# Kernel tuning notes

Measured on AMD Instinct MI355X. Metric: run time of the kernel, lower is better.

## Reference

```python
import jax, jax.numpy as jnp
import numpy as np

B, S, HID = 4, 2048, 768
NH = 12
HD = HID // NH  # 64


def setup_inputs() -> dict:
    key = jax.random.key(0)
    ks = jax.random.split(key, 8)
    scale = 1.0 / np.sqrt(HID)
    return {
        "hidden_states": jax.random.normal(ks[0], (B, S, HID), dtype=jnp.float32),
        "attention_mask": jnp.zeros((B, 1, 1, S), dtype=jnp.float32),
        "Wq": jax.random.normal(ks[1], (HID, HID), dtype=jnp.float32) * scale,
        "bq": jnp.zeros((HID,), dtype=jnp.float32),
        "Wk": jax.random.normal(ks[2], (HID, HID), dtype=jnp.float32) * scale,
        "bk": jnp.zeros((HID,), dtype=jnp.float32),
        "Wv": jax.random.normal(ks[3], (HID, HID), dtype=jnp.float32) * scale,
        "bv": jnp.zeros((HID,), dtype=jnp.float32),
    }


def _split_heads(x):
    # [B, S, HID] -> [B, NH, S, HD]
    return x.reshape(B, S, NH, HD).transpose(0, 2, 1, 3)


def reference(hidden_states, attention_mask, Wq, bq, Wk, bk, Wv, bv):
    q = _split_heads(hidden_states @ Wq + bq)
    k = _split_heads(hidden_states @ Wk + bk)
    v = _split_heads(hidden_states @ Wv + bv)
    # scores: [B, NH, S, S]
    scores = jnp.einsum("bhqd,bhkd->bhqk", q, k) / jnp.sqrt(jnp.float32(HD))
    scores = scores + attention_mask  # additive mask, broadcast [B,1,1,S]
    probs = jax.nn.softmax(scores, axis=-1)
    ctx = jnp.einsum("bhqk,bhkd->bhqd", probs, v)
    # [B, NH, S, HD] -> [B, S, HID]
    return ctx.transpose(0, 2, 1, 3).reshape(B, S, HID)
```

## Files before the change

kernel.cpp:

```cpp
#include <hip/hip_runtime.h>
#include <hip/hip_bf16.h>
#include <math.h>

#define B_ 4
#define S_ 2048
#define HID_ 768
#define NH_ 12
#define HD_ 64

typedef short bf16x8 __attribute__((ext_vector_type(8)));
typedef short bf16x4 __attribute__((ext_vector_type(4)));
typedef float f32x4 __attribute__((ext_vector_type(4)));
typedef unsigned short u16;
typedef unsigned int uu32;

#define QSCALE 0.18033688011112042f
#define LOG2E  1.4426950408889634f

__device__ __forceinline__ u16 f2bf(float f) {
  union { float f; unsigned u; } x; x.f = f;
  unsigned u = x.u;
  u += 0x7FFFu + ((u >> 16) & 1u);
  return (u16)(u >> 16);
}

__device__ __forceinline__ float exp2_fast(float x) {
  float r;
  asm("v_exp_f32 %0, %1" : "=v"(r) : "v"(x));
  return r;
}

__device__ __forceinline__ uu32 cvt_pk_bf16(float lo, float hi) {
  uu32 r;
  asm("v_cvt_pk_bf16_f32 %0, %1, %2" : "=v"(r) : "v"(lo), "v"(hi));
  return r;
}

__global__ void prep(const float* __restrict__ x, u16* __restrict__ xb,
                     const float* __restrict__ m, float* __restrict__ emf,
                     u16* __restrict__ emp,
                     const float* __restrict__ Wq, const float* __restrict__ Wk,
                     const float* __restrict__ Wv, u16* __restrict__ wt) {
  __shared__ float t[32][33];
  int bid = blockIdx.x;
  int tid = threadIdx.x;
  if (bid < 6144) {
    int i = (bid * 256 + tid) * 4;
    float4 v = *(const float4*)(x + i);
    ushort4 o;
    o.x = f2bf(v.x); o.y = f2bf(v.y); o.z = f2bf(v.z); o.w = f2bf(v.w);
    *(ushort4*)(xb + i) = o;
  } else if (bid < 6176) {
    int i = (bid - 6144) * 256 + tid;
    float e = exp2f(m[i] * LOG2E);
    emf[i] = e;
    int j = i & 63;
    int p = (j & 32) | (((j >> 2) & 3) << 3) | (((j >> 4) & 1) << 2) | (j & 3);
    emp[(i & ~63) | p] = f2bf(e);
  } else {
    int r = bid - 6176;
    int z = r / 576; r %= 576;
    int by = r / 24, bx = r % 24;
    const float* W = z == 0 ? Wq : (z == 1 ? Wk : Wv);
    u16* out = wt + (size_t)z * HID_ * HID_;
    int tx = tid & 31, ty = tid >> 5;
    int k0 = bx * 32, n0 = by * 32;
#pragma unroll
    for (int i = 0; i < 4; i++)
      t[ty + 8 * i][tx] = W[(k0 + ty + 8 * i) * HID_ + n0 + tx];
    __syncthreads();
#pragma unroll
    for (int i = 0; i < 4; i++)
      out[(n0 + ty + 8 * i) * HID_ + k0 + tx] = f2bf(t[tx][ty + 8 * i]);
  }
}

__global__ __launch_bounds__(256) void qkv_gemm4(
    const u16* __restrict__ xb, const u16* __restrict__ wt_all,
    const float* __restrict__ bq, const float* __restrict__ bk,
    const float* __restrict__ bv, const float* __restrict__ emf,
    u16* __restrict__ q, u16* __restrict__ k_, u16* __restrict__ vt) {
  int id = blockIdx.x;
  int xcd = id & 7, ii = id >> 3;
  int bx = xcd * 8 + (ii & 7);
  int by = ii >> 3;
  int z = by / 6;
  const float* bias = z == 0 ? bq : (z == 1 ? bk : bv);

  int tid = threadIdx.x;
  int l = tid & 63, w = tid >> 6;
  int lr = l & 15, lg = l >> 4;
  int wm = w >> 1, wn = w & 1;

  __shared__ __align__(16) u16 Al[2][128 * 40];
  __shared__ __align__(16) u16 Bl[2][128 * 40];

  const u16* Ab = xb + (size_t)bx * 128 * 768;
  const u16* Bb = wt_all + (size_t)by * 128 * 768;

  int sr = tid >> 1, sc = (tid & 1) * 2;
  const u16* ag = Ab + sr * 768 + sc * 8;
  const u16* bg = Bb + sr * 768 + sc * 8;
  int woff = sr * 40 + sc * 8;

  int aoff[4], boff[4];
#pragma unroll
  for (int mt = 0; mt < 4; mt++)
    aoff[mt] = (64 * wm + 16 * mt + lr) * 40 + lg * 8;
#pragma unroll
  for (int nt = 0; nt < 4; nt++)
    boff[nt] = (64 * wn + 16 * nt + lr) * 40 + lg * 8;

  bf16x8 sA0, sA1, sB0, sB1;

  sA0 = *(const bf16x8*)(ag);
  sA1 = *(const bf16x8*)(ag + 8);
  sB0 = *(const bf16x8*)(bg);
  sB1 = *(const bf16x8*)(bg + 8);
  *(bf16x8*)(&Al[0][woff]) = sA0;
  *(bf16x8*)(&Al[0][woff + 8]) = sA1;
  *(bf16x8*)(&Bl[0][woff]) = sB0;
  *(bf16x8*)(&Bl[0][woff + 8]) = sB1;
  __syncthreads();

  f32x4 acc[4][4] = {};

  auto body = [&](int buf, int t) {
    int k0 = (t + 1) * 32;
    sA0 = *(const bf16x8*)(ag + k0);
    sA1 = *(const bf16x8*)(ag + k0 + 8);
    sB0 = *(const bf16x8*)(bg + k0);
    sB1 = *(const bf16x8*)(bg + k0 + 8);

    bf16x8 af[4], bf[4];
#pragma unroll
    for (int mt = 0; mt < 4; mt++)
      af[mt] = *(const bf16x8*)(&Al[buf][aoff[mt]]);
#pragma unroll
    for (int nt = 0; nt < 4; nt++)
      bf[nt] = *(const bf16x8*)(&Bl[buf][boff[nt]]);
#pragma unroll
    for (int mt = 0; mt < 4; mt++)
#pragma unroll
      for (int nt = 0; nt < 4; nt++)
        acc[mt][nt] = __builtin_amdgcn_mfma_f32_16x16x32_bf16(af[mt], bf[nt], acc[mt][nt], 0, 0, 0);

    int nb = buf ^ 1;
    *(bf16x8*)(&Al[nb][woff]) = sA0;
    *(bf16x8*)(&Al[nb][woff + 8]) = sA1;
    *(bf16x8*)(&Bl[nb][woff]) = sB0;
    *(bf16x8*)(&Bl[nb][woff + 8]) = sB1;
    __syncthreads();
  };

#pragma unroll 1
  for (int tt = 0; tt < 11; ++tt) {
    body(0, 2 * tt);
    body(1, 2 * tt + 1);
  }
  body(0, 22);
  {
    bf16x8 af[4], bf[4];
#pragma unroll
    for (int mt = 0; mt < 4; mt++)
      af[mt] = *(const bf16x8*)(&Al[1][aoff[mt]]);
#pragma unroll
    for (int nt = 0; nt < 4; nt++)
      bf[nt] = *(const bf16x8*)(&Bl[1][boff[nt]]);
#pragma unroll
    for (int mt = 0; mt < 4; mt++)
#pragma unroll
      for (int nt = 0; nt < 4; nt++)
        acc[mt][nt] = __builtin_amdgcn_mfma_f32_16x16x32_bf16(af[mt], bf[nt], acc[mt][nt], 0, 0, 0);
  }

  int hh = 2 * (by % 6) + wn;
  int mbase = bx * 128 + 64 * wm;
  int bidx = mbase >> 11;
  float osc = z == 0 ? QSCALE : 1.0f;
#pragma unroll
  for (int mt = 0; mt < 4; mt++)
#pragma unroll
    for (int nt = 0; nt < 4; nt++) {
      int d = 16 * nt + lr;
      float bval = bias[(by % 6) * 128 + 64 * wn + d];
      int s = (mbase + 16 * mt + 4 * lg) & 2047;
      if (z == 2) {
        f32x4 emv = *(const f32x4*)(emf + (size_t)bidx * S_ + s);
        ushort4 pk;
        pk.x = f2bf((acc[mt][nt][0] + bval) * emv[0]);
        pk.y = f2bf((acc[mt][nt][1] + bval) * emv[1]);
        pk.z = f2bf((acc[mt][nt][2] + bval) * emv[2]);
        pk.w = f2bf((acc[mt][nt][3] + bval) * emv[3]);
        *(ushort4*)(vt + ((size_t)(bidx * NH_ + hh) * HD_ + d) * S_ + s) = pk;
      } else {
        u16* o = z == 0 ? q : k_;
#pragma unroll
        for (int r = 0; r < 4; r++)
          o[((size_t)(bidx * NH_ + hh) * S_ + s + r) * HD_ + d] =
              f2bf((acc[mt][nt][r] + bval) * osc);
      }
    }
}

__global__ __launch_bounds__(256) void attn9(
    const u16* __restrict__ q, const u16* __restrict__ k_,
    const u16* __restrict__ vt, const u16* __restrict__ emp,
    float* __restrict__ out) {
  int id = blockIdx.x;
  int xcd = id & 7, ii = id >> 3;
  int bh = xcd * 6 + (ii >> 4);
  int qb = ii & 15;
  int tid = threadIdx.x;
  int l = tid & 63, w = tid >> 6;
  int lr = l & 15, lg = l >> 4;
  int bidx = bh / NH_, h = bh % NH_;
  int q0 = qb * 128 + w * 32;

  __shared__ __align__(16) u16 Kl[2][64 * 64];
  __shared__ __align__(16) u16 Vl[2][64 * 64];
  __shared__ __align__(16) u16 El[2][16 * 64];

  {
    bf16x8 z = {};
    *(bf16x8*)(&El[0][0] + tid * 8) = z;
  }

  const u16* qbase = q + ((size_t)bh * S_ + q0) * HD_;
  const u16* kbase = k_ + (size_t)bh * S_ * HD_;
  const u16* vtb = vt + (size_t)bh * HD_ * S_;
  const u16* emb = emp + (size_t)bidx * S_;

  bf16x8 aq[2][2];
#pragma unroll
  for (int qt = 0; qt < 2; qt++)
#pragma unroll
    for (int h2 = 0; h2 < 2; h2++)
      aq[qt][h2] = *(const bf16x8*)(qbase + (size_t)(16 * qt + lr) * HD_ + 8 * lg + 32 * h2);

  f32x4 ctx[2][4] = {};
  f32x4 lsum[2] = {};

  int i0 = tid, i1 = tid + 256;
  int r0 = i0 >> 3, c0 = i0 & 7, r1 = i1 >> 3, c1 = i1 & 7;
  int kw0 = r0 * 64 + ((c0 ^ (r0 & 7)) << 3);
  int kw1 = r1 * 64 + ((c1 ^ (r1 & 7)) << 3);
  int w1_0 = 32 * (c0 >> 2) + 16 * (c0 & 1) + 4 * ((c0 >> 1) & 1);
  int w1_1 = 32 * (c1 >> 2) + 16 * (c1 & 1) + 4 * ((c1 >> 1) & 1);
  int vw0a = r0 * 64 + ((((w1_0 >> 3) ^ (r0 & 7)) << 3) | (w1_0 & 7));
  int vw0b = r0 * 64 + (((((w1_0 >> 3) + 1) ^ (r0 & 7)) << 3) | (w1_0 & 7));
  int vw1a = r1 * 64 + ((((w1_1 >> 3) ^ (r1 & 7)) << 3) | (w1_1 & 7));
  int vw1b = r1 * 64 + (((((w1_1 >> 3) + 1) ^ (r1 & 7)) << 3) | (w1_1 & 7));

  int sw = lr & 7;
  int off[4][2], eoff[2];
#pragma unroll
  for (int nt = 0; nt < 4; nt++)
#pragma unroll
    for (int hf = 0; hf < 2; hf++)
      off[nt][hf] = (16 * nt + lr) * 64 + (((hf * 4 + lg) ^ sw) << 3);
#pragma unroll
  for (int hf = 0; hf < 2; hf++)
    eoff[hf] = lr * 64 + (((hf * 4 + lg) ^ sw) << 3);

  bf16x8 sK0, sK1, sV0, sV1, sE;

  auto stage_load = [&](int kt) {
    const u16* kp = kbase + (size_t)kt * 64 * HD_;
    sK0 = *(const bf16x8*)(kp + i0 * 8);
    sK1 = *(const bf16x8*)(kp + i1 * 8);
    const u16* vp = vtb + kt * 64;
    sV0 = *(const bf16x8*)(vp + (size_t)r0 * S_ + c0 * 8);
    sV1 = *(const bf16x8*)(vp + (size_t)r1 * S_ + c1 * 8);
    if (tid < 8) sE = *(const bf16x8*)(emb + kt * 64 + tid * 8);
  };
  auto stage_write = [&](int buf) {
    u16* Kb = &Kl[buf][0];
    u16* Vb = &Vl[buf][0];
    *(bf16x8*)(Kb + kw0) = sK0;
    *(bf16x8*)(Kb + kw1) = sK1;
    union { bf16x8 v; bf16x4 hh[2]; } uv0, uv1;
    uv0.v = sV0; uv1.v = sV1;
    *(bf16x4*)(Vb + vw0a) = uv0.hh[0];
    *(bf16x4*)(Vb + vw0b) = uv0.hh[1];
    *(bf16x4*)(Vb + vw1a) = uv1.hh[0];
    *(bf16x4*)(Vb + vw1b) = uv1.hh[1];
    if (tid < 8) *(bf16x8*)(&El[buf][0] + tid * 8) = sE;
  };

  auto body = [&](int buf, int it) {
    stage_load((it + 1) & 31);

    const u16* Kp = &Kl[buf][0];
    const u16* Vp = &Vl[buf][0];
    const u16* Ep = &El[buf][0];

    bf16x8 kf[4][2];
#pragma unroll
    for (int nt = 0; nt < 4; nt++) {
      kf[nt][0] = *(const bf16x8*)(Kp + off[nt][0]);
      kf[nt][1] = *(const bf16x8*)(Kp + off[nt][1]);
    }

    f32x4 sc[2][4] = {};
    __builtin_amdgcn_s_setprio(1);
#pragma unroll
    for (int nt = 0; nt < 4; nt++)
#pragma unroll
      for (int qt = 0; qt < 2; qt++) {
        sc[qt][nt] = __builtin_amdgcn_mfma_f32_16x16x32_bf16(kf[nt][0], aq[qt][0], sc[qt][nt], 0, 0, 0);
        sc[qt][nt] = __builtin_amdgcn_mfma_f32_16x16x32_bf16(kf[nt][1], aq[qt][1], sc[qt][nt], 0, 0, 0);
      }
    __builtin_amdgcn_s_setprio(0);

    bf16x8 vf[4][2], ef[2];
#pragma unroll
    for (int nt = 0; nt < 4; nt++) {
      vf[nt][0] = *(const bf16x8*)(Vp + off[nt][0]);
      vf[nt][1] = *(const bf16x8*)(Vp + off[nt][1]);
    }
    ef[0] = *(const bf16x8*)(Ep + eoff[0]);
    ef[1] = *(const bf16x8*)(Ep + eoff[1]);

    union { bf16x8 v; uu32 u[4]; } pb[2][2];

#pragma unroll
    for (int qt = 0; qt < 2; qt++) {
#pragma unroll
      for (int nt = 0; nt < 4; nt++)
#pragma unroll
        for (int r = 0; r < 4; r++)
          sc[qt][nt][r] = exp2_fast(sc[qt][nt][r]);

#pragma unroll
      for (int h2 = 0; h2 < 2; h2++) {
        pb[qt][h2].u[0] = cvt_pk_bf16(sc[qt][2 * h2][0], sc[qt][2 * h2][1]);
        pb[qt][h2].u[1] = cvt_pk_bf16(sc[qt][2 * h2][2], sc[qt][2 * h2][3]);
        pb[qt][h2].u[2] = cvt_pk_bf16(sc[qt][2 * h2 + 1][0], sc[qt][2 * h2 + 1][1]);
        pb[qt][h2].u[3] = cvt_pk_bf16(sc[qt][2 * h2 + 1][2], sc[qt][2 * h2 + 1][3]);
      }

      lsum[qt] = __builtin_amdgcn_mfma_f32_16x16x32_bf16(ef[0], pb[qt][0].v, lsum[qt], 0, 0, 0);
      lsum[qt] = __builtin_amdgcn_mfma_f32_16x16x32_bf16(ef[1], pb[qt][1].v, lsum[qt], 0, 0, 0);
    }

    __builtin_amdgcn_s_setprio(1);
#pragma unroll
    for (int nt = 0; nt < 4; nt++)
#pragma unroll
      for (int qt = 0; qt < 2; qt++) {
        ctx[qt][nt] = __builtin_amdgcn_mfma_f32_16x16x32_bf16(vf[nt][0], pb[qt][0].v, ctx[qt][nt], 0, 0, 0);
        ctx[qt][nt] = __builtin_amdgcn_mfma_f32_16x16x32_bf16(vf[nt][1], pb[qt][1].v, ctx[qt][nt], 0, 0, 0);
      }
    __builtin_amdgcn_s_setprio(0);

    stage_write(buf ^ 1);
    __syncthreads();
  };

  stage_load(0);
  stage_write(0);
  __syncthreads();

  for (int t = 0; t < 16; ++t) {
    body(0, 2 * t);
    body(1, 2 * t + 1);
  }

  float* ct = (w < 2) ? ((float*)&Kl[0][0] + w * 1088)
                      : ((float*)&Vl[0][0] + (w - 2) * 1088);
#pragma unroll
  for (int qt = 0; qt < 2; qt++) {
    float den = __shfl(lsum[qt][0], lr);
    float inv = 1.f / den;
#pragma unroll
    for (int nt = 0; nt < 4; nt++) {
      f32x4 vv = ctx[qt][nt] * inv;
      *(f32x4*)(ct + lr * 68 + 16 * nt + 4 * lg) = vv;
    }
    __builtin_amdgcn_s_waitcnt(0);
    float* ob = out + ((size_t)bidx * S_ + q0 + 16 * qt) * HID_ + h * HD_;
#pragma unroll
    for (int i = 0; i < 16; i++)
      ob[(size_t)i * HID_ + l] = ct[i * 68 + l];
  }
}

extern "C" void kernel_launch(void* const* d_in, const int* in_sizes, int n_in,
                              void* d_out, int out_size, void* d_ws, size_t ws_size,
                              hipStream_t stream) {
  const float* x    = (const float*)d_in[0];
  const float* mask = (const float*)d_in[1];
  const float* Wq   = (const float*)d_in[2];
  const float* bq   = (const float*)d_in[3];
  const float* Wk   = (const float*)d_in[4];
  const float* bk   = (const float*)d_in[5];
  const float* Wv   = (const float*)d_in[6];
  const float* bv   = (const float*)d_in[7];
  float* out = (float*)d_out;

  char* ws = (char*)d_ws;
  const size_t SZ_X  = (size_t)B_ * S_ * HID_ * 2;
  const size_t SZ_W  = (size_t)3 * HID_ * HID_ * 2;
  u16* xb = (u16*)ws;
  u16* wt = (u16*)(ws + SZ_X);
  u16* q  = (u16*)(ws + SZ_X + SZ_W);
  u16* k  = (u16*)(ws + SZ_X + SZ_W + SZ_X);
  u16* vt = (u16*)(ws + SZ_X + SZ_W + 2 * SZ_X);
  float* emf = (float*)(ws + SZ_X + SZ_W + 3 * SZ_X);
  u16* emp = (u16*)(ws + SZ_X + SZ_W + 3 * SZ_X + (size_t)B_ * S_ * 4);

  hipLaunchKernelGGL(prep, dim3(7904), dim3(256), 0, stream,
                     x, xb, mask, emf, emp, Wq, Wk, Wv, wt);
  hipLaunchKernelGGL(qkv_gemm4, dim3(1152), dim3(256), 0, stream,
                     xb, wt, bq, bk, bv, emf, q, k, vt);
  hipLaunchKernelGGL(attn9, dim3(768), dim3(256), 0, stream, q, k, vt, emp, out);
}
```

Measured before the change: 124.4 us.

## Fuse fp32-to-bf16 activation conversion into QKV GEMM loads; drop attention setprio

The separate prep pass that converted hidden_states to bf16 is removed. The QKV GEMM now reads fp32 activations directly and converts them to bf16 with packed converts before writing to shared memory. This avoids a full write and re-read of a bf16 copy of x, but the GEMM now reads twice as many bytes per A tile, and each of the 18 column-block tiles re-reads that fp32 data. Separately, the s_setprio calls around the MFMA sections in the attention kernel are removed.

```diff
diff --git a/kernel.cpp b/kernel.cpp
--- a/kernel.cpp
+++ b/kernel.cpp
@@ -36,29 +36,22 @@
   return r;
 }
 
-__global__ void prep(const float* __restrict__ x, u16* __restrict__ xb,
-                     const float* __restrict__ m, float* __restrict__ emf,
+__global__ void prep(const float* __restrict__ m, float* __restrict__ emf,
                      u16* __restrict__ emp,
                      const float* __restrict__ Wq, const float* __restrict__ Wk,
                      const float* __restrict__ Wv, u16* __restrict__ wt) {
   __shared__ float t[32][33];
   int bid = blockIdx.x;
   int tid = threadIdx.x;
-  if (bid < 6144) {
-    int i = (bid * 256 + tid) * 4;
-    float4 v = *(const float4*)(x + i);
-    ushort4 o;
-    o.x = f2bf(v.x); o.y = f2bf(v.y); o.z = f2bf(v.z); o.w = f2bf(v.w);
-    *(ushort4*)(xb + i) = o;
-  } else if (bid < 6176) {
-    int i = (bid - 6144) * 256 + tid;
+  if (bid < 32) {
+    int i = bid * 256 + tid;
     float e = exp2f(m[i] * LOG2E);
     emf[i] = e;
     int j = i & 63;
     int p = (j & 32) | (((j >> 2) & 3) << 3) | (((j >> 4) & 1) << 2) | (j & 3);
     emp[(i & ~63) | p] = f2bf(e);
   } else {
-    int r = bid - 6176;
+    int r = bid - 32;
     int z = r / 576; r %= 576;
     int by = r / 24, bx = r % 24;
     const float* W = z == 0 ? Wq : (z == 1 ? Wk : Wv);
@@ -75,8 +68,8 @@
   }
 }
 
-__global__ __launch_bounds__(256) void qkv_gemm4(
-    const u16* __restrict__ xb, const u16* __restrict__ wt_all,
+__global__ __launch_bounds__(256) void qkv_gemm5(
+    const float* __restrict__ x, const u16* __restrict__ wt_all,
     const float* __restrict__ bq, const float* __restrict__ bk,
     const float* __restrict__ bv, const float* __restrict__ emf,
     u16* __restrict__ q, u16* __restrict__ k_, u16* __restrict__ vt) {
@@ -95,11 +88,10 @@
   __shared__ __align__(16) u16 Al[2][128 * 40];
   __shared__ __align__(16) u16 Bl[2][128 * 40];
 
-  const u16* Ab = xb + (size_t)bx * 128 * 768;
   const u16* Bb = wt_all + (size_t)by * 128 * 768;
 
   int sr = tid >> 1, sc = (tid & 1) * 2;
-  const u16* ag = Ab + sr * 768 + sc * 8;
+  const float* ag = x + (size_t)bx * 128 * 768 + sr * 768 + sc * 8;
   const u16* bg = Bb + sr * 768 + sc * 8;
   int woff = sr * 40 + sc * 8;
 
@@ -111,24 +103,42 @@
   for (int nt = 0; nt < 4; nt++)
     boff[nt] = (64 * wn + 16 * nt + lr) * 40 + lg * 8;
 
-  bf16x8 sA0, sA1, sB0, sB1;
-
-  sA0 = *(const bf16x8*)(ag);
-  sA1 = *(const bf16x8*)(ag + 8);
+  f32x4 rA0, rA1, rA2, rA3;
+  bf16x8 sB0, sB1;
+
+  auto loadA = [&](int k0) {
+    rA0 = *(const f32x4*)(ag + k0);
+    rA1 = *(const f32x4*)(ag + k0 + 4);
+    rA2 = *(const f32x4*)(ag + k0 + 8);
+    rA3 = *(const f32x4*)(ag + k0 + 12);
+  };
+  auto writeTile = [&](int buf) {
+    union { bf16x8 v; uu32 u[4]; } p0, p1;
+    p0.u[0] = cvt_pk_bf16(rA0[0], rA0[1]);
+    p0.u[1] = cvt_pk_bf16(rA0[2], rA0[3]);
+    p0.u[2] = cvt_pk_bf16(rA1[0], rA1[1]);
+    p0.u[3] = cvt_pk_bf16(rA1[2], rA1[3]);
+    p1.u[0] = cvt_pk_bf16(rA2[0], rA2[1]);
+    p1.u[1] = cvt_pk_bf16(rA2[2], rA2[3]);
+    p1.u[2] = cvt_pk_bf16(rA3[0], rA3[1]);
+    p1.u[3] = cvt_pk_bf16(rA3[2], rA3[3]);
+    *(bf16x8*)(&Al[buf][woff]) = p0.v;
+    *(bf16x8*)(&Al[buf][woff + 8]) = p1.v;
+    *(bf16x8*)(&Bl[buf][woff]) = sB0;
+    *(bf16x8*)(&Bl[buf][woff + 8]) = sB1;
+  };
+
+  loadA(0);
   sB0 = *(const bf16x8*)(bg);
   sB1 = *(const bf16x8*)(bg + 8);
-  *(bf16x8*)(&Al[0][woff]) = sA0;
-  *(bf16x8*)(&Al[0][woff + 8]) = sA1;
-  *(bf16x8*)(&Bl[0][woff]) = sB0;
-  *(bf16x8*)(&Bl[0][woff + 8]) = sB1;
+  writeTile(0);
   __syncthreads();
 
   f32x4 acc[4][4] = {};
 
   auto body = [&](int buf, int t) {
     int k0 = (t + 1) * 32;
-    sA0 = *(const bf16x8*)(ag + k0);
-    sA1 = *(const bf16x8*)(ag + k0 + 8);
+    loadA(k0);
     sB0 = *(const bf16x8*)(bg + k0);
     sB1 = *(const bf16x8*)(bg + k0 + 8);
 
@@ -145,11 +155,7 @@
       for (int nt = 0; nt < 4; nt++)
         acc[mt][nt] = __builtin_amdgcn_mfma_f32_16x16x32_bf16(af[mt], bf[nt], acc[mt][nt], 0, 0, 0);
 
-    int nb = buf ^ 1;
-    *(bf16x8*)(&Al[nb][woff]) = sA0;
-    *(bf16x8*)(&Al[nb][woff + 8]) = sA1;
-    *(bf16x8*)(&Bl[nb][woff]) = sB0;
-    *(bf16x8*)(&Bl[nb][woff + 8]) = sB1;
+    writeTile(buf ^ 1);
     __syncthreads();
   };
 
@@ -203,7 +209,7 @@
     }
 }
 
-__global__ __launch_bounds__(256) void attn9(
+__global__ __launch_bounds__(256) void attn10(
     const u16* __restrict__ q, const u16* __restrict__ k_,
     const u16* __restrict__ vt, const u16* __restrict__ emp,
     float* __restrict__ out) {
@@ -303,7 +309,6 @@
     }
 
     f32x4 sc[2][4] = {};
-    __builtin_amdgcn_s_setprio(1);
 #pragma unroll
     for (int nt = 0; nt < 4; nt++)
 #pragma unroll
@@ -311,7 +316,6 @@
         sc[qt][nt] = __builtin_amdgcn_mfma_f32_16x16x32_bf16(kf[nt][0], aq[qt][0], sc[qt][nt], 0, 0, 0);
         sc[qt][nt] = __builtin_amdgcn_mfma_f32_16x16x32_bf16(kf[nt][1], aq[qt][1], sc[qt][nt], 0, 0, 0);
       }
-    __builtin_amdgcn_s_setprio(0);
 
     bf16x8 vf[4][2], ef[2];
 #pragma unroll
@@ -344,7 +348,6 @@
       lsum[qt] = __builtin_amdgcn_mfma_f32_16x16x32_bf16(ef[1], pb[qt][1].v, lsum[qt], 0, 0, 0);
     }
 
-    __builtin_amdgcn_s_setprio(1);
 #pragma unroll
     for (int nt = 0; nt < 4; nt++)
 #pragma unroll
@@ -352,7 +355,6 @@
         ctx[qt][nt] = __builtin_amdgcn_mfma_f32_16x16x32_bf16(vf[nt][0], pb[qt][0].v, ctx[qt][nt], 0, 0, 0);
         ctx[qt][nt] = __builtin_amdgcn_mfma_f32_16x16x32_bf16(vf[nt][1], pb[qt][1].v, ctx[qt][nt], 0, 0, 0);
       }
-    __builtin_amdgcn_s_setprio(0);
 
     stage_write(buf ^ 1);
     __syncthreads();
@@ -402,17 +404,16 @@
   char* ws = (char*)d_ws;
   const size_t SZ_X  = (size_t)B_ * S_ * HID_ * 2;
   const size_t SZ_W  = (size_t)3 * HID_ * HID_ * 2;
-  u16* xb = (u16*)ws;
-  u16* wt = (u16*)(ws + SZ_X);
-  u16* q  = (u16*)(ws + SZ_X + SZ_W);
-  u16* k  = (u16*)(ws + SZ_X + SZ_W + SZ_X);
-  u16* vt = (u16*)(ws + SZ_X + SZ_W + 2 * SZ_X);
-  float* emf = (float*)(ws + SZ_X + SZ_W + 3 * SZ_X);
-  u16* emp = (u16*)(ws + SZ_X + SZ_W + 3 * SZ_X + (size_t)B_ * S_ * 4);
-
-  hipLaunchKernelGGL(prep, dim3(7904), dim3(256), 0, stream,
-                     x, xb, mask, emf, emp, Wq, Wk, Wv, wt);
-  hipLaunchKernelGGL(qkv_gemm4, dim3(1152), dim3(256), 0, stream,
-                     xb, wt, bq, bk, bv, emf, q, k, vt);
-  hipLaunchKernelGGL(attn9, dim3(768), dim3(256), 0, stream, q, k, vt, emp, out);
-}
+  u16* wt = (u16*)ws;
+  u16* q  = (u16*)(ws + SZ_W);
+  u16* k  = (u16*)(ws + SZ_W + SZ_X);
+  u16* vt = (u16*)(ws + SZ_W + 2 * SZ_X);
+  float* emf = (float*)(ws + SZ_W + 3 * SZ_X);
+  u16* emp = (u16*)(ws + SZ_W + 3 * SZ_X + (size_t)B_ * S_ * 4);
+
+  hipLaunchKernelGGL(prep, dim3(1760), dim3(256), 0, stream,
+                     mask, emf, emp, Wq, Wk, Wv, wt);
+  hipLaunchKernelGGL(qkv_gemm5, dim3(1152), dim3(256), 0, stream,
+                     x, wt, bq, bk, bv, emf, q, k, vt);
+  hipLaunchKernelGGL(attn10, dim3(768), dim3(256), 0, stream, q, k, vt, emp, out);
+}
```

Measured after the change: 132.6 us. 6.6% more time.

## Fold attention mask into score MFMA accumulator instead of scaling V

Applied to the files above, without the earlier changes.

The additive mask (times log2e) is now loaded per key tile and passed as the initial accumulator of the QK^T MFMA. Previously exp(mask) multiplied V and also fed the row-sum MFMA through an LDS tile. This removes the LDS mask staging, the emf multiply in the V epilogue and the per-tile E loads, and uses a constant ones-column operand for the row-sum. It also pads the GEMM LDS row stride from 40 to 44 and drops the s_setprio hints. In exchange, each tile now does extra global float4 loads of mask values per lane, and large negative masks now flow through exp2 rather than a zero multiply.

```diff
diff --git a/kernel.cpp b/kernel.cpp
--- a/kernel.cpp
+++ b/kernel.cpp
@@ -37,8 +37,7 @@
 }
 
 __global__ void prep(const float* __restrict__ x, u16* __restrict__ xb,
-                     const float* __restrict__ m, float* __restrict__ emf,
-                     u16* __restrict__ emp,
+                     const float* __restrict__ m, float* __restrict__ mskl,
                      const float* __restrict__ Wq, const float* __restrict__ Wk,
                      const float* __restrict__ Wv, u16* __restrict__ wt) {
   __shared__ float t[32][33];
@@ -52,11 +51,7 @@
     *(ushort4*)(xb + i) = o;
   } else if (bid < 6176) {
     int i = (bid - 6144) * 256 + tid;
-    float e = exp2f(m[i] * LOG2E);
-    emf[i] = e;
-    int j = i & 63;
-    int p = (j & 32) | (((j >> 2) & 3) << 3) | (((j >> 4) & 1) << 2) | (j & 3);
-    emp[(i & ~63) | p] = f2bf(e);
+    mskl[i] = m[i] * LOG2E;
   } else {
     int r = bid - 6176;
     int z = r / 576; r %= 576;
@@ -75,10 +70,10 @@
   }
 }
 
-__global__ __launch_bounds__(256) void qkv_gemm4(
+__global__ __launch_bounds__(256) void qkv_gemm6(
     const u16* __restrict__ xb, const u16* __restrict__ wt_all,
     const float* __restrict__ bq, const float* __restrict__ bk,
-    const float* __restrict__ bv, const float* __restrict__ emf,
+    const float* __restrict__ bv,
     u16* __restrict__ q, u16* __restrict__ k_, u16* __restrict__ vt) {
   int id = blockIdx.x;
   int xcd = id & 7, ii = id >> 3;
@@ -92,8 +87,8 @@
   int lr = l & 15, lg = l >> 4;
   int wm = w >> 1, wn = w & 1;
 
-  __shared__ __align__(16) u16 Al[2][128 * 40];
-  __shared__ __align__(16) u16 Bl[2][128 * 40];
+  __shared__ __align__(16) u16 Al[2][128 * 44];
+  __shared__ __align__(16) u16 Bl[2][128 * 44];
 
   const u16* Ab = xb + (size_t)bx * 128 * 768;
   const u16* Bb = wt_all + (size_t)by * 128 * 768;
@@ -101,15 +96,15 @@
   int sr = tid >> 1, sc = (tid & 1) * 2;
   const u16* ag = Ab + sr * 768 + sc * 8;
   const u16* bg = Bb + sr * 768 + sc * 8;
-  int woff = sr * 40 + sc * 8;
+  int woff = sr * 44 + sc * 8;
 
   int aoff[4], boff[4];
 #pragma unroll
   for (int mt = 0; mt < 4; mt++)
-    aoff[mt] = (64 * wm + 16 * mt + lr) * 40 + lg * 8;
+    aoff[mt] = (64 * wm + 16 * mt + lr) * 44 + lg * 8;
 #pragma unroll
   for (int nt = 0; nt < 4; nt++)
-    boff[nt] = (64 * wn + 16 * nt + lr) * 40 + lg * 8;
+    boff[nt] = (64 * wn + 16 * nt + lr) * 44 + lg * 8;
 
   bf16x8 sA0, sA1, sB0, sB1;
 
@@ -186,12 +181,11 @@
       float bval = bias[(by % 6) * 128 + 64 * wn + d];
       int s = (mbase + 16 * mt + 4 * lg) & 2047;
       if (z == 2) {
-        f32x4 emv = *(const f32x4*)(emf + (size_t)bidx * S_ + s);
         ushort4 pk;
-        pk.x = f2bf((acc[mt][nt][0] + bval) * emv[0]);
-        pk.y = f2bf((acc[mt][nt][1] + bval) * emv[1]);
-        pk.z = f2bf((acc[mt][nt][2] + bval) * emv[2]);
-        pk.w = f2bf((acc[mt][nt][3] + bval) * emv[3]);
+        pk.x = f2bf(acc[mt][nt][0] + bval);
+        pk.y = f2bf(acc[mt][nt][1] + bval);
+        pk.z = f2bf(acc[mt][nt][2] + bval);
+        pk.w = f2bf(acc[mt][nt][3] + bval);
         *(ushort4*)(vt + ((size_t)(bidx * NH_ + hh) * HD_ + d) * S_ + s) = pk;
       } else {
         u16* o = z == 0 ? q : k_;
@@ -203,9 +197,9 @@
     }
 }
 
-__global__ __launch_bounds__(256) void attn9(
+__global__ __launch_bounds__(256) void attn11(
     const u16* __restrict__ q, const u16* __restrict__ k_,
-    const u16* __restrict__ vt, const u16* __restrict__ emp,
+    const u16* __restrict__ vt, const float* __restrict__ mskl,
     float* __restrict__ out) {
   int id = blockIdx.x;
   int xcd = id & 7, ii = id >> 3;
@@ -219,17 +213,11 @@
 
   __shared__ __align__(16) u16 Kl[2][64 * 64];
   __shared__ __align__(16) u16 Vl[2][64 * 64];
-  __shared__ __align__(16) u16 El[2][16 * 64];
-
-  {
-    bf16x8 z = {};
-    *(bf16x8*)(&El[0][0] + tid * 8) = z;
-  }
 
   const u16* qbase = q + ((size_t)bh * S_ + q0) * HD_;
   const u16* kbase = k_ + (size_t)bh * S_ * HD_;
   const u16* vtb = vt + (size_t)bh * HD_ * S_;
-  const u16* emb = emp + (size_t)bidx * S_;
+  const float* mrow = mskl + (size_t)bidx * S_;
 
   bf16x8 aq[2][2];
 #pragma unroll
@@ -237,6 +225,13 @@
 #pragma unroll
     for (int h2 = 0; h2 < 2; h2++)
       aq[qt][h2] = *(const bf16x8*)(qbase + (size_t)(16 * qt + lr) * HD_ + 8 * lg + 32 * h2);
+
+  bf16x8 efc;
+  {
+    u16 ov = (lr == 0) ? (u16)0x3F80 : (u16)0;
+#pragma unroll
+    for (int j = 0; j < 8; j++) efc[j] = (short)ov;
+  }
 
   f32x4 ctx[2][4] = {};
   f32x4 lsum[2] = {};
@@ -253,17 +248,14 @@
   int vw1b = r1 * 64 + (((((w1_1 >> 3) + 1) ^ (r1 & 7)) << 3) | (w1_1 & 7));
 
   int sw = lr & 7;
-  int off[4][2], eoff[2];
+  int off[4][2];
 #pragma unroll
   for (int nt = 0; nt < 4; nt++)
 #pragma unroll
     for (int hf = 0; hf < 2; hf++)
       off[nt][hf] = (16 * nt + lr) * 64 + (((hf * 4 + lg) ^ sw) << 3);
-#pragma unroll
-  for (int hf = 0; hf < 2; hf++)
-    eoff[hf] = lr * 64 + (((hf * 4 + lg) ^ sw) << 3);
-
-  bf16x8 sK0, sK1, sV0, sV1, sE;
+
+  bf16x8 sK0, sK1, sV0, sV1;
 
   auto stage_load = [&](int kt) {
     const u16* kp = kbase + (size_t)kt * 64 * HD_;
@@ -272,7 +264,6 @@
     const u16* vp = vtb + kt * 64;
     sV0 = *(const bf16x8*)(vp + (size_t)r0 * S_ + c0 * 8);
     sV1 = *(const bf16x8*)(vp + (size_t)r1 * S_ + c1 * 8);
-    if (tid < 8) sE = *(const bf16x8*)(emb + kt * 64 + tid * 8);
   };
   auto stage_write = [&](int buf) {
     u16* Kb = &Kl[buf][0];
@@ -285,15 +276,19 @@
     *(bf16x4*)(Vb + vw0b) = uv0.hh[1];
     *(bf16x4*)(Vb + vw1a) = uv1.hh[0];
     *(bf16x4*)(Vb + vw1b) = uv1.hh[1];
-    if (tid < 8) *(bf16x8*)(&El[buf][0] + tid * 8) = sE;
   };
 
   auto body = [&](int buf, int it) {
+    int kb = it * 64;
     stage_load((it + 1) & 31);
+
+    f32x4 mk4[4];
+#pragma unroll
+    for (int nt = 0; nt < 4; nt++)
+      mk4[nt] = *(const f32x4*)(mrow + kb + 16 * nt + 4 * lg);
 
     const u16* Kp = &Kl[buf][0];
     const u16* Vp = &Vl[buf][0];
-    const u16* Ep = &El[buf][0];
 
     bf16x8 kf[4][2];
 #pragma unroll
@@ -302,25 +297,21 @@
       kf[nt][1] = *(const bf16x8*)(Kp + off[nt][1]);
     }
 
-    f32x4 sc[2][4] = {};
-    __builtin_amdgcn_s_setprio(1);
+    f32x4 sc[2][4];
 #pragma unroll
     for (int nt = 0; nt < 4; nt++)
 #pragma unroll
       for (int qt = 0; qt < 2; qt++) {
-        sc[qt][nt] = __builtin_amdgcn_mfma_f32_16x16x32_bf16(kf[nt][0], aq[qt][0], sc[qt][nt], 0, 0, 0);
+        sc[qt][nt] = __builtin_amdgcn_mfma_f32_16x16x32_bf16(kf[nt][0], aq[qt][0], mk4[nt], 0, 0, 0);
         sc[qt][nt] = __builtin_amdgcn_mfma_f32_16x16x32_bf16(kf[nt][1], aq[qt][1], sc[qt][nt], 0, 0, 0);
       }
-    __builtin_amdgcn_s_setprio(0);
-
-    bf16x8 vf[4][2], ef[2];
+
+    bf16x8 vf[4][2];
 #pragma unroll
     for (int nt = 0; nt < 4; nt++) {
       vf[nt][0] = *(const bf16x8*)(Vp + off[nt][0]);
       vf[nt][1] = *(const bf16x8*)(Vp + off[nt][1]);
     }
-    ef[0] = *(const bf16x8*)(Ep + eoff[0]);
-    ef[1] = *(const bf16x8*)(Ep + eoff[1]);
 
     union { bf16x8 v; uu32 u[4]; } pb[2][2];
 
@@ -340,11 +331,10 @@
         pb[qt][h2].u[3] = cvt_pk_bf16(sc[qt][2 * h2 + 1][2], sc[qt][2 * h2 + 1][3]);
       }
 
-      lsum[qt] = __builtin_amdgcn_mfma_f32_16x16x32_bf16(ef[0], pb[qt][0].v, lsum[qt], 0, 0, 0);
-      lsum[qt] = __builtin_amdgcn_mfma_f32_16x16x32_bf16(ef[1], pb[qt][1].v, lsum[qt], 0, 0, 0);
+      lsum[qt] = __builtin_amdgcn_mfma_f32_16x16x32_bf16(efc, pb[qt][0].v, lsum[qt], 0, 0, 0);
+      lsum[qt] = __builtin_amdgcn_mfma_f32_16x16x32_bf16(efc, pb[qt][1].v, lsum[qt], 0, 0, 0);
     }
 
-    __builtin_amdgcn_s_setprio(1);
 #pragma unroll
     for (int nt = 0; nt < 4; nt++)
 #pragma unroll
@@ -352,7 +342,6 @@
         ctx[qt][nt] = __builtin_amdgcn_mfma_f32_16x16x32_bf16(vf[nt][0], pb[qt][0].v, ctx[qt][nt], 0, 0, 0);
         ctx[qt][nt] = __builtin_amdgcn_mfma_f32_16x16x32_bf16(vf[nt][1], pb[qt][1].v, ctx[qt][nt], 0, 0, 0);
       }
-    __builtin_amdgcn_s_setprio(0);
 
     stage_write(buf ^ 1);
     __syncthreads();
@@ -407,12 +396,11 @@
   u16* q  = (u16*)(ws + SZ_X + SZ_W);
   u16* k  = (u16*)(ws + SZ_X + SZ_W + SZ_X);
   u16* vt = (u16*)(ws + SZ_X + SZ_W + 2 * SZ_X);
-  float* emf = (float*)(ws + SZ_X + SZ_W + 3 * SZ_X);
-  u16* emp = (u16*)(ws + SZ_X + SZ_W + 3 * SZ_X + (size_t)B_ * S_ * 4);
+  float* mskl = (float*)(ws + SZ_X + SZ_W + 3 * SZ_X);
 
   hipLaunchKernelGGL(prep, dim3(7904), dim3(256), 0, stream,
-                     x, xb, mask, emf, emp, Wq, Wk, Wv, wt);
-  hipLaunchKernelGGL(qkv_gemm4, dim3(1152), dim3(256), 0, stream,
-                     xb, wt, bq, bk, bv, emf, q, k, vt);
-  hipLaunchKernelGGL(attn9, dim3(768), dim3(256), 0, stream, q, k, vt, emp, out);
-}
+                     x, xb, mask, mskl, Wq, Wk, Wv, wt);
+  hipLaunchKernelGGL(qkv_gemm6, dim3(1152), dim3(256), 0, stream,
+                     xb, wt, bq, bk, bv, q, k, vt);
+  hipLaunchKernelGGL(attn11, dim3(768), dim3(256), 0, stream, q, k, vt, mskl, out);
+}
```

After: 148.3 us. +19.2%, slower.
